# Optimization experiments

Measured on AMD Instinct MI355X. Metric: run time of the kernel, lower is better.

## Reference

```python
import jax, jax.numpy as jnp
import numpy as np

B, S, H_IN, H = 32, 1024, 1024, 1024


def setup_inputs() -> dict:
    key = jax.random.key(0)
    k1, k2, k3, k4, k5, k6, k7 = jax.random.split(key, 7)
    hidden = jax.random.normal(k1, (B, H), dtype=jnp.float32)
    encoder_outputs = jax.random.normal(k2, (S, B, H_IN), dtype=jnp.float32)
    mask = jax.random.randint(k3, (B, S), 0, 2).astype(bool)
    mask = mask.at[:, 0].set(False)  # ensure at least one unmasked position per row
    lim1 = 1.0 / np.sqrt(H_IN + H)
    lim2 = 1.0 / np.sqrt(H)
    W1 = jax.random.uniform(k4, (H, H_IN + H), minval=-lim1, maxval=lim1, dtype=jnp.float32)
    b1 = jax.random.uniform(k5, (H,), minval=-lim1, maxval=lim1, dtype=jnp.float32)
    W2 = jax.random.uniform(k6, (1, H), minval=-lim2, maxval=lim2, dtype=jnp.float32)
    b2 = jax.random.uniform(k7, (1,), minval=-lim2, maxval=lim2, dtype=jnp.float32)
    return {"hidden": hidden, "encoder_outputs": encoder_outputs, "mask": mask,
            "W1": W1, "b1": b1, "W2": W2, "b2": b2}


def reference(hidden, encoder_outputs, mask, W1, b1, W2, b2):
    # encoder_outputs: [S,B,Hin] -> [B,S,Hin]; hidden: [B,H] broadcast over S.
    enc = jnp.transpose(encoder_outputs, (1, 0, 2))  # [B,S,Hin]
    # cat([enc, hidden], -1) @ W1.T == enc @ W1_enc.T + hidden @ W1_hid.T (avoids materializing concat)
    W1_enc, W1_hid = W1[:, :enc.shape[-1]], W1[:, enc.shape[-1]:]
    a1 = jnp.einsum('bsi,hi->bsh', enc, W1_enc) + (hidden @ W1_hid.T)[:, None, :] + b1
    a1 = jnp.tanh(a1)                                # [B,S,H]
    scores = jnp.einsum('bsh,h->bs', a1, W2[0]) + b2[0]  # [B,S]
    scores = jnp.where(mask, -jnp.inf, scores)
    attn = jax.nn.softmax(scores, axis=-1)           # softmax over seq dim
    return attn[:, None, :]                          # [B,1,S]
```

## Files before the change

### kernel.cpp

```cpp
#include <hip/hip_runtime.h>
#include <hip/hip_bf16.h>
#include <cstdint>


#define BK 64
#define NKT 16

typedef short  s16x8 __attribute__((ext_vector_type(8)));
typedef float  f32x4 __attribute__((ext_vector_type(4)));
typedef unsigned int u32;
typedef unsigned short u16;
typedef unsigned long long u64;

__device__ static inline u32 f2bf(float f) {
    u32 u = __float_as_uint(f);
    return (u + 0x7fffu + ((u >> 16) & 1u)) >> 16;
}
__device__ static inline u32 pk2(float a, float b) {
    return f2bf(a) | (f2bf(b) << 16);
}

__device__ static inline void gload_lds16(const void* g, void* l) {
    __builtin_amdgcn_global_load_lds(
        (const __attribute__((address_space(1))) u32*)g,
        (__attribute__((address_space(3))) u32*)l, 16, 0, 0);
}

__global__ __launch_bounds__(256) void prep_k(const float* __restrict__ W1,
                                              const float* __restrict__ hidden,
                                              const float* __restrict__ b1,
                                              const void*  __restrict__ maskv,
                                              u16*   __restrict__ Wb,
                                              float* __restrict__ hv,
                                              int*   __restrict__ sidx,
                                              int*   __restrict__ cnt,
                                              float* __restrict__ scores) {
    const int bx = blockIdx.x, t = threadIdx.x;
    const int wid = t >> 6, lane = t & 63;
    __shared__ int sflag[4];

    if (bx < 512) {
        const int i = bx * 256 + t;
        const int n = i >> 7, gc = i & 127;
        const int p = (gc & ~7) | ((gc & 7) ^ (n & 7));
        const float4 v0 = *(const float4*)(W1 + (size_t)n * 2048 + gc * 8);
        const float4 v1 = *(const float4*)(W1 + (size_t)n * 2048 + gc * 8 + 4);
        uint4 o; o.x = pk2(v0.x, v0.y); o.y = pk2(v0.z, v0.w);
        o.z = pk2(v1.x, v1.y); o.w = pk2(v1.z, v1.w);
        *(uint4*)(Wb + (size_t)n * 1024 + p * 8) = o;
    } else if (bx < 768) {
        const int h = (bx - 512) * 4 + wid;
        const float4* wrow = (const float4*)(W1 + (size_t)h * 2048 + 1024);
        float4 w[4];
#pragma unroll
        for (int q = 0; q < 4; q++) w[q] = wrow[lane + 64 * q];
        for (int b = 0; b < 32; b++) {
            const float4* hb = (const float4*)(hidden + (size_t)b * 1024);
            float p = 0.f;
#pragma unroll
            for (int q = 0; q < 4; q++) {
                float4 x = hb[lane + 64 * q];
                p = fmaf(w[q].x, x.x, fmaf(w[q].y, x.y, fmaf(w[q].z, x.z, fmaf(w[q].w, x.w, p))));
            }
#pragma unroll
            for (int off = 1; off < 64; off <<= 1) p += __shfl_xor(p, off);
            if (lane == 0) hv[(size_t)b * 1024 + h] = p + b1[h];
        }
    } else if (bx < 776) {
        const u32* mw = (const u32*)maskv;
        int f = 0;
#pragma unroll
        for (int j = 0; j < 32; j++) f |= (mw[t * 32 + j] > 1u) ? 1 : 0;
        const int anyf = __any(f);
        if (lane == 0) sflag[wid] = anyf;
        __syncthreads();
        const int bytemode = sflag[0] | sflag[1] | sflag[2] | sflag[3];

        const int b = (bx - 768) * 4 + wid;
        int base = 0;
        for (int c = 0; c < 16; c++) {
            const int s = c * 64 + lane;
            int m;
            if (bytemode) m = ((const unsigned char*)maskv)[(size_t)b * 1024 + s];
            else          m = ((const int*)maskv)[(size_t)b * 1024 + s];
            const u64 bal = __ballot(m == 0);
            if (m == 0) {
                const int off = (int)__popcll(bal & ((1ull << lane) - 1ull));
                sidx[(size_t)b * 1024 + base + off] = s;
            }
            base += (int)__popcll(bal);
        }
        if (lane == 0) cnt[b] = base;
        for (int j = base + lane; j < 1024; j += 64) sidx[(size_t)b * 1024 + j] = 0;
    } else {
        const int i = (bx - 776) * 256 + t;
        ((float4*)scores)[i] = make_float4(0.f, 0.f, 0.f, 0.f);
    }
}

__global__ __launch_bounds__(256) void conv_k(const float* __restrict__ enc,
                                              const int* __restrict__ sidx,
                                              const int* __restrict__ cnt,
                                              u16* __restrict__ encC) {
    const int bid = blockIdx.x, t = threadIdx.x;
    const int xcd = bid & 7, w = bid >> 3;
    const int b = xcd * 4 + (w >> 8);
    const int j0 = (w & 255) * 4;
    const int c = cnt[b];
    if (j0 >= ((c + 127) & ~127)) return;
    const int gc = t >> 1, h = t & 1;
#pragma unroll
    for (int r = 0; r < 4; r++) {
        const int j = j0 + r;
        const int s = (j < c) ? sidx[(size_t)b * 1024 + j] : 0;
        const float4 v = ((const float4*)(enc + ((size_t)s * 32 + b) * 1024))[t];
        const int p = (gc & ~7) | ((gc & 7) ^ (j & 7));
        uint2 o; o.x = pk2(v.x, v.y); o.y = pk2(v.z, v.w);
        *(uint2*)(encC + ((size_t)b * 1024 + j) * 1024 + p * 8 + h * 4) = o;
    }
}

__global__ __launch_bounds__(256, 6) void gemm_s(
    const u16* __restrict__ encC,
    const u16* __restrict__ Wb,
    const int* __restrict__ sidx,
    const int* __restrict__ cnt,
    const float* __restrict__ hv,
    const float* __restrict__ W2,
    float*      __restrict__ scores)
{
    __shared__ u16 As[64 * BK];
    __shared__ u16 Bs[128 * BK];

    const int tid = threadIdx.x;
    const int bid = blockIdx.x;
    const int xcd = bid & 7, idx = bid >> 3;
    const int strip = xcd * 64 + (idx >> 3);
    const int nt = idx & 7;
    const int b = strip >> 4, mt = strip & 15;
    const int c = cnt[b];
    if (mt * 64 >= c) return;

    const int srow = tid >> 3, sc16 = tid & 7;
    const u16* asrc = encC + ((size_t)b * 1024 + mt * 64 + srow) * 1024 + sc16 * 8;
    const u16* bsrc = Wb + ((size_t)(nt * 128) + srow) * 1024 + sc16 * 8;

    const int wid = tid >> 6, lane = tid & 63;
    const int wr = wid >> 1, wc = wid & 1;
    const int lhi = lane >> 4, llo = lane & 15;

    f32x4 acc[2][4] = {};

    for (int kt = 0; kt < NKT; kt++) {
        const size_t ko = (size_t)kt * 64;
#pragma unroll
        for (int j = 0; j < 2; j++)
            gload_lds16(asrc + ko + (size_t)j * 32 * 1024, &As[(j * 256 + tid) * 8]);
#pragma unroll
        for (int j = 0; j < 4; j++)
            gload_lds16(bsrc + ko + (size_t)j * 32 * 1024, &Bs[(j * 256 + tid) * 8]);
        __syncthreads();
#pragma unroll
        for (int kk = 0; kk < 2; kk++) {
            s16x8 af[2], bfr[4];
#pragma unroll
            for (int f = 0; f < 2; f++) {
                const int row = wr * 32 + f * 16 + llo;
                const int ph = (kk * 4 + lhi) ^ (llo & 7);
                af[f] = *(const s16x8*)&As[row * BK + ph * 8];
            }
#pragma unroll
            for (int f = 0; f < 4; f++) {
                const int row = wc * 64 + f * 16 + llo;
                const int ph = (kk * 4 + lhi) ^ (llo & 7);
                bfr[f] = *(const s16x8*)&Bs[row * BK + ph * 8];
            }
#pragma unroll
            for (int fi = 0; fi < 2; fi++)
#pragma unroll
                for (int fj = 0; fj < 4; fj++)
                    acc[fi][fj] = __builtin_amdgcn_mfma_f32_16x16x32_bf16(af[fi], bfr[fj], acc[fi][fj], 0, 0, 0);
        }
        __syncthreads();
    }

    const float* hvb = hv + (size_t)b * 1024;
    float hvv[4], w2v[4];
#pragma unroll
    for (int fj = 0; fj < 4; fj++) {
        const int n = nt * 128 + wc * 64 + fj * 16 + llo;
        hvv[fj] = hvb[n];
        w2v[fj] = W2[n];
    }
#pragma unroll
    for (int fi = 0; fi < 2; fi++) {
#pragma unroll
        for (int r = 0; r < 4; r++) {
            float sum = 0.f;
#pragma unroll
            for (int fj = 0; fj < 4; fj++) {
                const float x = acc[fi][fj][r] + hvv[fj];
                const float e = __expf(2.f * x);
                const float t = 1.f - 2.f / (e + 1.f);
                sum = fmaf(t, w2v[fj], sum);
            }
            sum += __shfl_xor(sum, 1);
            sum += __shfl_xor(sum, 2);
            sum += __shfl_xor(sum, 4);
            sum += __shfl_xor(sum, 8);
            if (llo == 0) {
                const int j = mt * 64 + wr * 32 + fi * 16 + lhi * 4 + r;
                if (j < c) {
                    const int s = sidx[(size_t)b * 1024 + j];
                    atomicAdd(&scores[(size_t)b * 1024 + s], sum);
                }
            }
        }
    }
}

__global__ __launch_bounds__(256) void softmax_k(const float* __restrict__ scores,
                                                 const void* __restrict__ maskv,
                                                 float* __restrict__ out) {
    const int b = blockIdx.x, t = threadIdx.x;
    const int wid = t >> 6, lane = t & 63;
    const u32* mw = (const u32*)maskv;
    int f = 0;
#pragma unroll
    for (int j = 0; j < 32; j++) f |= (mw[t * 32 + j] > 1u) ? 1 : 0;
    __shared__ int sflag[4];
    const int anyf = __any(f);
    if (lane == 0) sflag[wid] = anyf;
    __syncthreads();
    const int bytemode = sflag[0] | sflag[1] | sflag[2] | sflag[3];

    int m0, m1, m2, m3;
    if (bytemode) {
        const uchar4 mk = ((const uchar4*)((const unsigned char*)maskv + (size_t)b * 1024))[t];
        m0 = mk.x; m1 = mk.y; m2 = mk.z; m3 = mk.w;
    } else {
        const int4 mk = ((const int4*)((const int*)maskv + (size_t)b * 1024))[t];
        m0 = mk.x; m1 = mk.y; m2 = mk.z; m3 = mk.w;
    }
    const float4 sc = ((const float4*)(scores + (size_t)b * 1024))[t];
    const float v0 = m0 ? -1e30f : sc.x;
    const float v1 = m1 ? -1e30f : sc.y;
    const float v2 = m2 ? -1e30f : sc.z;
    const float v3 = m3 ? -1e30f : sc.w;
    float mx = fmaxf(fmaxf(v0, v1), fmaxf(v2, v3));
#pragma unroll
    for (int off = 1; off < 64; off <<= 1) mx = fmaxf(mx, __shfl_xor(mx, off));
    __shared__ float redm[4], reds[4];
    if (lane == 0) redm[wid] = mx;
    __syncthreads();
    mx = fmaxf(fmaxf(redm[0], redm[1]), fmaxf(redm[2], redm[3]));
    const float e0 = m0 ? 0.f : __expf(v0 - mx);
    const float e1 = m1 ? 0.f : __expf(v1 - mx);
    const float e2 = m2 ? 0.f : __expf(v2 - mx);
    const float e3 = m3 ? 0.f : __expf(v3 - mx);
    float s = e0 + e1 + e2 + e3;
#pragma unroll
    for (int off = 1; off < 64; off <<= 1) s += __shfl_xor(s, off);
    if (lane == 0) reds[wid] = s;
    __syncthreads();
    s = reds[0] + reds[1] + reds[2] + reds[3];
    const float inv = 1.f / s;
    float4 o; o.x = e0 * inv; o.y = e1 * inv; o.z = e2 * inv; o.w = e3 * inv;
    ((float4*)(out + (size_t)b * 1024))[t] = o;
}

extern "C" void kernel_launch(void* const* d_in, const int* in_sizes, int n_in,
                              void* d_out, int out_size, void* d_ws, size_t ws_size,
                              hipStream_t stream) {
    const float* hidden = (const float*)d_in[0];
    const float* enc    = (const float*)d_in[1];
    const void*  mask   = d_in[2];
    const float* W1 = (const float*)d_in[3];
    const float* b1 = (const float*)d_in[4];
    const float* W2 = (const float*)d_in[5];
    float* out = (float*)d_out;

    char* ws = (char*)d_ws;
    float* ws_scores = (float*)ws;
    float* ws_hv     = (float*)(ws + (128u << 10));
    u16*   ws_Wb     = (u16*)(ws + (256u << 10));
    int*   ws_cnt    = (int*)(ws + (2304u << 10));
    int*   ws_sidx   = (int*)(ws + (2432u << 10));
    u16*   ws_encC   = (u16*)(ws + (4096u << 10));

    prep_k<<<808, 256, 0, stream>>>(W1, hidden, b1, mask, ws_Wb, ws_hv, ws_sidx, ws_cnt, ws_scores);
    conv_k<<<8192, 256, 0, stream>>>(enc, ws_sidx, ws_cnt, ws_encC);
    gemm_s<<<4096, 256, 0, stream>>>(ws_encC, ws_Wb, ws_sidx, ws_cnt, ws_hv, W2, ws_scores);
    softmax_k<<<32, 256, 0, stream>>>(ws_scores, mask, out);
}
```

Measured before the change: 101.5 us.

## Store encoder bf16 in MFMA fragment layout and load A directly to registers

The conversion kernel now writes the compacted bf16 encoder rows in a pre-swizzled fragment order that matches the MFMA operand layout. The GEMM kernel drops the shared-memory A tile and loads each A fragment with one 16-byte global load per lane. This removes the LDS staging traffic and bank pressure for A. In exchange, A reads go through global memory and L2 without software prefetch, which could expose load latency in the k-loop.

```diff
diff --git a/kernel.cpp b/kernel.cpp
--- a/kernel.cpp
+++ b/kernel.cpp
@@ -101,27 +101,33 @@
 __global__ __launch_bounds__(256) void conv_k(const float* __restrict__ enc,
                                               const int* __restrict__ sidx,
                                               const int* __restrict__ cnt,
-                                              u16* __restrict__ encC) {
+                                              u16* __restrict__ encF) {
     const int bid = blockIdx.x, t = threadIdx.x;
     const int xcd = bid & 7, w = bid >> 3;
     const int b = xcd * 4 + (w >> 8);
     const int j0 = (w & 255) * 4;
     const int c = cnt[b];
     if (j0 >= ((c + 127) & ~127)) return;
-    const int gc = t >> 1, h = t & 1;
-#pragma unroll
-    for (int r = 0; r < 4; r++) {
-        const int j = j0 + r;
+#pragma unroll
+    for (int p = 0; p < 2; p++) {
+        const int q = t + p * 256;
+        const int jl = q >> 7, c8 = q & 127;
+        const int j = j0 + jl;
         const int s = (j < c) ? sidx[(size_t)b * 1024 + j] : 0;
-        const float4 v = ((const float4*)(enc + ((size_t)s * 32 + b) * 1024))[t];
-        const int p = (gc & ~7) | ((gc & 7) ^ (j & 7));
-        uint2 o; o.x = pk2(v.x, v.y); o.y = pk2(v.z, v.w);
-        *(uint2*)(encC + ((size_t)b * 1024 + j) * 1024 + p * 8 + h * 4) = o;
-    }
-}
-
-__global__ __launch_bounds__(256, 6) void gemm_s(
-    const u16* __restrict__ encC,
+        const float* src = enc + ((size_t)s * 32 + b) * 1024 + c8 * 8;
+        const float4 v0 = *(const float4*)src;
+        const float4 v1 = *(const float4*)(src + 4);
+        const int rt = j >> 4, llo = j & 15;
+        const int kt = c8 >> 3, kk = (c8 >> 2) & 1, lhi = c8 & 3;
+        const size_t a16 = (((size_t)b * 64 + rt) * 32 + kt * 2 + kk) * 64 + lhi * 16 + llo;
+        uint4 o; o.x = pk2(v0.x, v0.y); o.y = pk2(v0.z, v0.w);
+        o.z = pk2(v1.x, v1.y); o.w = pk2(v1.z, v1.w);
+        *(uint4*)(encF + a16 * 8) = o;
+    }
+}
+
+__global__ __launch_bounds__(256, 6) void gemm_h(
+    const u16* __restrict__ encF,
     const u16* __restrict__ Wb,
     const int* __restrict__ sidx,
     const int* __restrict__ cnt,
@@ -129,7 +135,6 @@
     const float* __restrict__ W2,
     float*      __restrict__ scores)
 {
-    __shared__ u16 As[64 * BK];
     __shared__ u16 Bs[128 * BK];
 
     const int tid = threadIdx.x;
@@ -141,34 +146,30 @@
     const int c = cnt[b];
     if (mt * 64 >= c) return;
 
-    const int srow = tid >> 3, sc16 = tid & 7;
-    const u16* asrc = encC + ((size_t)b * 1024 + mt * 64 + srow) * 1024 + sc16 * 8;
-    const u16* bsrc = Wb + ((size_t)(nt * 128) + srow) * 1024 + sc16 * 8;
-
     const int wid = tid >> 6, lane = tid & 63;
     const int wr = wid >> 1, wc = wid & 1;
     const int lhi = lane >> 4, llo = lane & 15;
 
+    const u16* Abase = encF + (((size_t)b * 64 + mt * 4 + wr * 2) * 32 * 64 + lane) * 8;
+
+    const int srow = tid >> 3, sc16 = tid & 7;
+    const u16* bsrc = Wb + ((size_t)(nt * 128) + srow) * 1024 + sc16 * 8;
+
     f32x4 acc[2][4] = {};
 
     for (int kt = 0; kt < NKT; kt++) {
         const size_t ko = (size_t)kt * 64;
-#pragma unroll
-        for (int j = 0; j < 2; j++)
-            gload_lds16(asrc + ko + (size_t)j * 32 * 1024, &As[(j * 256 + tid) * 8]);
 #pragma unroll
         for (int j = 0; j < 4; j++)
             gload_lds16(bsrc + ko + (size_t)j * 32 * 1024, &Bs[(j * 256 + tid) * 8]);
         __syncthreads();
 #pragma unroll
         for (int kk = 0; kk < 2; kk++) {
+            const int aoff = (kt * 2 + kk) * 512;
             s16x8 af[2], bfr[4];
 #pragma unroll
-            for (int f = 0; f < 2; f++) {
-                const int row = wr * 32 + f * 16 + llo;
-                const int ph = (kk * 4 + lhi) ^ (llo & 7);
-                af[f] = *(const s16x8*)&As[row * BK + ph * 8];
-            }
+            for (int fi = 0; fi < 2; fi++)
+                af[fi] = *(const s16x8*)(Abase + aoff + fi * 16384);
 #pragma unroll
             for (int f = 0; f < 4; f++) {
                 const int row = wc * 64 + f * 16 + llo;
@@ -179,7 +180,8 @@
             for (int fi = 0; fi < 2; fi++)
 #pragma unroll
                 for (int fj = 0; fj < 4; fj++)
-                    acc[fi][fj] = __builtin_amdgcn_mfma_f32_16x16x32_bf16(af[fi], bfr[fj], acc[fi][fj], 0, 0, 0);
+                    acc[fi][fj] = __builtin_amdgcn_mfma_f32_16x16x32_bf16(
+                        af[fi], bfr[fj], acc[fi][fj], 0, 0, 0);
         }
         __syncthreads();
     }
@@ -286,10 +288,10 @@
     u16*   ws_Wb     = (u16*)(ws + (256u << 10));
     int*   ws_cnt    = (int*)(ws + (2304u << 10));
     int*   ws_sidx   = (int*)(ws + (2432u << 10));
-    u16*   ws_encC   = (u16*)(ws + (4096u << 10));
+    u16*   ws_encF   = (u16*)(ws + (4096u << 10));
 
     prep_k<<<808, 256, 0, stream>>>(W1, hidden, b1, mask, ws_Wb, ws_hv, ws_sidx, ws_cnt, ws_scores);
-    conv_k<<<8192, 256, 0, stream>>>(enc, ws_sidx, ws_cnt, ws_encC);
-    gemm_s<<<4096, 256, 0, stream>>>(ws_encC, ws_Wb, ws_sidx, ws_cnt, ws_hv, W2, ws_scores);
+    conv_k<<<8192, 256, 0, stream>>>(enc, ws_sidx, ws_cnt, ws_encF);
+    gemm_h<<<4096, 256, 0, stream>>>(ws_encF, ws_Wb, ws_sidx, ws_cnt, ws_hv, W2, ws_scores);
     softmax_k<<<32, 256, 0, stream>>>(ws_scores, mask, out);
 }
```

Measured after the change: 118.0 us. 16.3% more time.
